# Optimization experiments

Measured on AMD Instinct MI355X. Metric: run time of the kernel, lower is better.

## Reference

```python
import jax, jax.numpy as jnp
import numpy as np

N, D, F, E, K = 8192, 1024, 4096, 8, 2


def setup_inputs() -> dict:
    key = jax.random.key(0)
    ks = jax.random.split(key, 4)
    x = jax.random.normal(ks[0], (N, D), dtype=jnp.float32)
    Wg = jax.random.normal(ks[1], (D, E), dtype=jnp.float32) * 0.02
    W1 = jax.random.normal(ks[2], (E, D, F), dtype=jnp.float32) * 0.02
    b1 = jnp.zeros((E, F), dtype=jnp.float32)
    W2 = jax.random.normal(ks[3], (E, F, D), dtype=jnp.float32) * 0.02
    b2 = jnp.zeros((E, D), dtype=jnp.float32)
    return {"x": x, "Wg": Wg, "W1": W1, "b1": b1, "W2": W2, "b2": b2}


def reference(x, Wg, W1, b1, W2, b2):
    # Top-k softmax gate (TopKGate): pick K experts per token, renormalize.
    logits = x @ Wg                                        # [N, E]
    probs = jax.nn.softmax(logits, axis=-1)
    gate_vals, expert_idx = jax.lax.top_k(probs, K)        # [N, K]
    gate_w = gate_vals / jnp.sum(gate_vals, axis=-1, keepdims=True)

    # Expert FFN (dispatch/combine math): the torch code sorts tokens by expert
    # id, all-to-alls them to the owning rank, applies the local Expert MLP,
    # and combines back weighted by gate_w. The jit-friendly equivalent is to
    # compute every expert's MLP for all tokens and gather the selected rows.
    h = jax.nn.relu(jnp.einsum('nd,edf->enf', x, W1) + b1[:, None, :])  # [E, N, F]
    o = jnp.einsum('enf,efd->end', h, W2) + b2[:, None, :]               # [E, N, D]

    tok = jnp.arange(x.shape[0])
    sel = o[expert_idx, tok[:, None]]                      # [N, K, D]
    y = jnp.sum(gate_w[..., None] * sel, axis=1)           # [N, D]
    return y
```

## Files before the change

kernel.cpp:

```cpp
#include <hip/hip_runtime.h>

#define N_TOK 8192
#define DIM   1024
#define FFN   4096
#define NEXP  8
#define TOPK  2
#define NENT  (N_TOK * TOPK)

using short8  = __attribute__((ext_vector_type(8))) short;
using floatx4 = __attribute__((ext_vector_type(4))) float;

__device__ __forceinline__ unsigned short f2bf(float f) {
    union { float f; unsigned u; } v; v.f = f;
    unsigned r = v.u + 0x7fffu + ((v.u >> 16) & 1u);
    return (unsigned short)(r >> 16);
}

#define GLOAD_LDS16(gptr, lptr) __builtin_amdgcn_global_load_lds( \
    (__attribute__((address_space(1))) void*)(void*)(gptr),       \
    (__attribute__((address_space(3))) void*)(lptr), 16, 0, 0)


__global__ __launch_bounds__(256) void cvt_x_kernel(const float4* __restrict__ in,
                                                    ushort4* __restrict__ out) {
    int i = blockIdx.x * 256 + threadIdx.x;
    float4 v = in[i];
    ushort4 o;
    o.x = f2bf(v.x); o.y = f2bf(v.y); o.z = f2bf(v.z); o.w = f2bf(v.w);
    out[i] = o;
}

__global__ __launch_bounds__(256) void transpose_cvt(const float* __restrict__ in,
                                                     unsigned short* __restrict__ out,
                                                     int R, int C) {
    __shared__ float tile[32][33];
    int e  = blockIdx.z;
    int c0 = blockIdx.x * 32;
    int r0 = blockIdx.y * 32;
    const float* inp = in + (size_t)e * R * C;
    unsigned short* outp = out + (size_t)e * R * C;
    int tx = threadIdx.x, ty = threadIdx.y;
#pragma unroll
    for (int i = 0; i < 4; i++) {
        int r = ty + i * 8;
        tile[r][tx] = inp[(size_t)(r0 + r) * C + c0 + tx];
    }
    __syncthreads();
#pragma unroll
    for (int i = 0; i < 4; i++) {
        int c = ty + i * 8;
        outp[(size_t)(c0 + c) * R + r0 + tx] = f2bf(tile[tx][c]);
    }
}


__global__ __launch_bounds__(256) void gating_kernel(const float* __restrict__ x,
                                                     const float* __restrict__ wg,
                                                     int* __restrict__ topk_e,
                                                     float* __restrict__ topk_w,
                                                     int* __restrict__ counts) {
    int wave = threadIdx.x >> 6, lane = threadIdx.x & 63;
    int t = blockIdx.x * 4 + wave;
    const float* xr = x + (size_t)t * DIM;
    float acc[NEXP];
#pragma unroll
    for (int e = 0; e < NEXP; e++) acc[e] = 0.f;
    for (int it = 0; it < DIM / 64; it++) {
        int d = it * 64 + lane;
        float xv = xr[d];
        const float4* wr = (const float4*)(wg + d * NEXP);
        float4 w0 = wr[0], w1 = wr[1];
        acc[0] += xv * w0.x; acc[1] += xv * w0.y; acc[2] += xv * w0.z; acc[3] += xv * w0.w;
        acc[4] += xv * w1.x; acc[5] += xv * w1.y; acc[6] += xv * w1.z; acc[7] += xv * w1.w;
    }
#pragma unroll
    for (int e = 0; e < NEXP; e++) {
#pragma unroll
        for (int off = 32; off > 0; off >>= 1) acc[e] += __shfl_xor(acc[e], off);
    }
    if (lane == 0) {
        int e1 = 0; float l1 = acc[0];
        for (int e = 1; e < NEXP; e++) if (acc[e] > l1) { l1 = acc[e]; e1 = e; }
        int e2 = -1; float l2 = -3.4e38f;
        for (int e = 0; e < NEXP; e++) if (e != e1 && acc[e] > l2) { l2 = acc[e]; e2 = e; }
        float w1v = 1.f / (1.f + expf(l2 - l1));
        topk_e[t * 2]     = e1;  topk_e[t * 2 + 1] = e2;
        topk_w[t * 2]     = w1v; topk_w[t * 2 + 1] = 1.f - w1v;
        atomicAdd(&counts[e1], 1);
        atomicAdd(&counts[e2], 1);
    }
}

__global__ void prefix_kernel(const int* __restrict__ counts, int* __restrict__ offs) {
    if (threadIdx.x == 0) {
        int s = 0;
        for (int e = 0; e < NEXP; e++) { offs[e] = s; s += counts[e]; }
        offs[NEXP] = s;
    }
}

__global__ __launch_bounds__(256) void scatter_kernel(const int* __restrict__ topk_e,
                                                      const float* __restrict__ topk_w,
                                                      const int* __restrict__ offs,
                                                      int* __restrict__ cursors,
                                                      int* __restrict__ entry_token,
                                                      float* __restrict__ entry_wgt) {
    int t = blockIdx.x * 256 + threadIdx.x;
#pragma unroll
    for (int k = 0; k < TOPK; k++) {
        int e = topk_e[t * 2 + k];
        int pos = offs[e] + atomicAdd(&cursors[e], 1);
        entry_token[pos] = t;
        entry_wgt[pos]  = topk_w[t * 2 + k];
    }
}


__global__ __launch_bounds__(256) void gemm1_kernel(
    const unsigned short* __restrict__ xb,
    const unsigned short* __restrict__ w1t,
    const float* __restrict__ b1,
    const int* __restrict__ offs,
    const int* __restrict__ entry_token,
    unsigned short* __restrict__ h)
{
    int e    = blockIdx.z;
    int base = offs[e];
    int cnt  = offs[e + 1] - base;
    int m0   = blockIdx.y * 128;
    if (m0 >= cnt) return;
    int f0   = blockIdx.x * 128;

    __shared__ unsigned short As[128 * 32];
    __shared__ unsigned short Bs[128 * 32];
    __shared__ int toks[128];

    int tid = threadIdx.x;
    if (tid < 128) {
        int r = m0 + tid;
        toks[tid] = entry_token[base + (r < cnt ? r : 0)];
    }
    __syncthreads();

    int wave = tid >> 6, lane = tid & 63;
    int wm = (wave >> 1) * 64, wn = (wave & 1) * 64;

    int rA   = wave * 32 + (lane >> 2);
    int colg = (lane & 3) * 8;
    const unsigned short* aG0 = xb + (size_t)toks[rA] * DIM + colg;
    const unsigned short* aG1 = xb + (size_t)toks[rA + 16] * DIM + colg;
    const unsigned short* bG0 = w1t + ((size_t)e * FFN + f0 + rA) * DIM + colg;
    const unsigned short* bG1 = bG0 + (size_t)16 * DIM;
    unsigned short* ldsA0 = &As[wave * 1024];
    unsigned short* ldsA1 = &As[wave * 1024 + 512];
    unsigned short* ldsB0 = &Bs[wave * 1024];
    unsigned short* ldsB1 = &Bs[wave * 1024 + 512];

    floatx4 acc[4][4];
#pragma unroll
    for (int i = 0; i < 4; i++)
#pragma unroll
        for (int j = 0; j < 4; j++) acc[i][j] = (floatx4)0.f;

    int quad = lane >> 4, rm = lane & 15;
    int aoff = (wm + rm) * 32 + quad * 8;
    int boff = (wn + rm) * 32 + quad * 8;

    for (int kk = 0; kk < DIM / 32; kk++) {
        GLOAD_LDS16(aG0, ldsA0);
        GLOAD_LDS16(aG1, ldsA1);
        GLOAD_LDS16(bG0, ldsB0);
        GLOAD_LDS16(bG1, ldsB1);
        aG0 += 32; aG1 += 32; bG0 += 32; bG1 += 32;
        __syncthreads();
        short8 af[4], bfr[4];
#pragma unroll
        for (int mi = 0; mi < 4; mi++) af[mi] = *(const short8*)&As[aoff + mi * 512];
#pragma unroll
        for (int ni = 0; ni < 4; ni++) bfr[ni] = *(const short8*)&Bs[boff + ni * 512];
#pragma unroll
        for (int mi = 0; mi < 4; mi++)
#pragma unroll
            for (int ni = 0; ni < 4; ni++)
                acc[mi][ni] = __builtin_amdgcn_mfma_f32_16x16x32_bf16(af[mi], bfr[ni], acc[mi][ni], 0, 0, 0);
        __syncthreads();
    }

#pragma unroll
    for (int mi = 0; mi < 4; mi++) {
        int mbase = wm + mi * 16 + quad * 4;
#pragma unroll
        for (int ni = 0; ni < 4; ni++) {
            int f = f0 + wn + ni * 16 + rm;
            float bias = b1[e * FFN + f];
            floatx4 v = acc[mi][ni];
#pragma unroll
            for (int r = 0; r < 4; r++) {
                int row = m0 + mbase + r;
                if (row < cnt) {
                    float t = v[r] + bias;
                    t = t > 0.f ? t : 0.f;
                    h[(size_t)(base + row) * FFN + f] = f2bf(t);
                }
            }
        }
    }
}


__global__ __launch_bounds__(256) void gemm2_kernel(
    const unsigned short* __restrict__ h,
    const unsigned short* __restrict__ w2t,
    const float* __restrict__ b2,
    const int* __restrict__ offs,
    const int* __restrict__ entry_token,
    const float* __restrict__ entry_wgt,
    float* __restrict__ y)
{
    int e    = blockIdx.z;
    int base = offs[e];
    int cnt  = offs[e + 1] - base;
    int m0   = blockIdx.y * 128;
    if (m0 >= cnt) return;
    int n0   = blockIdx.x * 128;

    __shared__ unsigned short As[128 * 32];
    __shared__ unsigned short Bs[128 * 32];

    int tid = threadIdx.x;
    int wave = tid >> 6, lane = tid & 63;
    int wm = (wave >> 1) * 64, wn = (wave & 1) * 64;

    int rA   = wave * 32 + (lane >> 2);
    int colg = (lane & 3) * 8;
    const unsigned short* aG0 = h + (size_t)(base + m0 + rA) * FFN + colg;
    const unsigned short* aG1 = aG0 + (size_t)16 * FFN;
    const unsigned short* bG0 = w2t + ((size_t)e * DIM + n0 + rA) * FFN + colg;
    const unsigned short* bG1 = bG0 + (size_t)16 * FFN;
    unsigned short* ldsA0 = &As[wave * 1024];
    unsigned short* ldsA1 = &As[wave * 1024 + 512];
    unsigned short* ldsB0 = &Bs[wave * 1024];
    unsigned short* ldsB1 = &Bs[wave * 1024 + 512];

    floatx4 acc[4][4];
#pragma unroll
    for (int i = 0; i < 4; i++)
#pragma unroll
        for (int j = 0; j < 4; j++) acc[i][j] = (floatx4)0.f;

    int quad = lane >> 4, rm = lane & 15;
    int aoff = (wm + rm) * 32 + quad * 8;
    int boff = (wn + rm) * 32 + quad * 8;

    for (int kk = 0; kk < FFN / 32; kk++) {
        GLOAD_LDS16(aG0, ldsA0);
        GLOAD_LDS16(aG1, ldsA1);
        GLOAD_LDS16(bG0, ldsB0);
        GLOAD_LDS16(bG1, ldsB1);
        aG0 += 32; aG1 += 32; bG0 += 32; bG1 += 32;
        __syncthreads();
        short8 af[4], bfr[4];
#pragma unroll
        for (int mi = 0; mi < 4; mi++) af[mi] = *(const short8*)&As[aoff + mi * 512];
#pragma unroll
        for (int ni = 0; ni < 4; ni++) bfr[ni] = *(const short8*)&Bs[boff + ni * 512];
#pragma unroll
        for (int mi = 0; mi < 4; mi++)
#pragma unroll
            for (int ni = 0; ni < 4; ni++)
                acc[mi][ni] = __builtin_amdgcn_mfma_f32_16x16x32_bf16(af[mi], bfr[ni], acc[mi][ni], 0, 0, 0);
        __syncthreads();
    }

#pragma unroll
    for (int mi = 0; mi < 4; mi++) {
        int mbase = wm + mi * 16 + quad * 4;
#pragma unroll
        for (int ni = 0; ni < 4; ni++) {
            int n = n0 + wn + ni * 16 + rm;
            float bias = b2[e * DIM + n];
            floatx4 v = acc[mi][ni];
#pragma unroll
            for (int r = 0; r < 4; r++) {
                int row = m0 + mbase + r;
                if (row < cnt) {
                    int   tok = entry_token[base + row];
                    float w   = entry_wgt[base + row];
                    atomicAdd(&y[(size_t)tok * DIM + n], (v[r] + bias) * w);
                }
            }
        }
    }
}


extern "C" void kernel_launch(void* const* d_in, const int* in_sizes, int n_in,
                              void* d_out, int out_size, void* d_ws, size_t ws_size,
                              hipStream_t stream) {
    const float* x  = (const float*)d_in[0];
    const float* Wg = (const float*)d_in[1];
    const float* W1 = (const float*)d_in[2];
    const float* b1 = (const float*)d_in[3];
    const float* W2 = (const float*)d_in[4];
    const float* b2 = (const float*)d_in[5];
    float* y = (float*)d_out;

    char* p = (char*)d_ws;
    unsigned short* xb  = (unsigned short*)p; p += (size_t)N_TOK * DIM * 2;
    unsigned short* w1t = (unsigned short*)p; p += (size_t)NEXP * DIM * FFN * 2;
    unsigned short* w2t = (unsigned short*)p; p += (size_t)NEXP * DIM * FFN * 2;
    unsigned short* h   = (unsigned short*)p; p += (size_t)(NENT + 128) * FFN * 2;
    int*   topk_e      = (int*)p;   p += (size_t)N_TOK * TOPK * 4;
    float* topk_w      = (float*)p; p += (size_t)N_TOK * TOPK * 4;
    int*   entry_token = (int*)p;   p += (size_t)NENT * 4;
    float* entry_wgt   = (float*)p; p += (size_t)NENT * 4;
    int*   counts      = (int*)p;   p += NEXP * 4;
    int*   cursors     = (int*)p;   p += NEXP * 4;
    int*   offs        = (int*)p;   p += (NEXP + 1) * 4;

    hipMemsetAsync(d_out, 0, (size_t)out_size * 4, stream);
    hipMemsetAsync(counts, 0, NEXP * 4 * 2, stream);

    cvt_x_kernel<<<(N_TOK * DIM) / (256 * 4), 256, 0, stream>>>((const float4*)x, (ushort4*)xb);
    transpose_cvt<<<dim3(FFN / 32, DIM / 32, NEXP), dim3(32, 8), 0, stream>>>(W1, w1t, DIM, FFN);
    transpose_cvt<<<dim3(DIM / 32, FFN / 32, NEXP), dim3(32, 8), 0, stream>>>(W2, w2t, FFN, DIM);
    gating_kernel<<<N_TOK / 4, 256, 0, stream>>>(x, Wg, topk_e, topk_w, counts);
    prefix_kernel<<<1, 64, 0, stream>>>(counts, offs);
    scatter_kernel<<<N_TOK / 256, 256, 0, stream>>>(topk_e, topk_w, offs, cursors, entry_token, entry_wgt);
    gemm1_kernel<<<dim3(FFN / 128, 64, NEXP), 256, 0, stream>>>(xb, w1t, b1, offs, entry_token, h);
    gemm2_kernel<<<dim3(DIM / 128, 64, NEXP), 256, 0, stream>>>(h, w2t, b2, offs, entry_token, entry_wgt, y);
}
```

Measured before the change: 1.128 ms.

## Double K-tile depth to 64 with XOR-swizzled LDS layout in both expert GEMMs

Both expert GEMMs now stage a 64-wide K slice per iteration instead of 32, which halves the number of barrier pairs per tile. The LDS layout uses an XOR swizzle on 16-byte chunks so the MFMA fragment reads avoid bank conflicts. The weight transpose kernel now handles 64 rows per block and writes packed ushort2 stores for wider writes. This costs twice the LDS per block, which may lower occupancy.

```diff
diff --git a/kernel.cpp b/kernel.cpp
--- a/kernel.cpp
+++ b/kernel.cpp
@@ -33,23 +33,26 @@
 __global__ __launch_bounds__(256) void transpose_cvt(const float* __restrict__ in,
                                                      unsigned short* __restrict__ out,
                                                      int R, int C) {
-    __shared__ float tile[32][33];
+    __shared__ float tile[64][33];
     int e  = blockIdx.z;
     int c0 = blockIdx.x * 32;
-    int r0 = blockIdx.y * 32;
+    int r0 = blockIdx.y * 64;
     const float* inp = in + (size_t)e * R * C;
     unsigned short* outp = out + (size_t)e * R * C;
     int tx = threadIdx.x, ty = threadIdx.y;
 #pragma unroll
+    for (int i = 0; i < 8; i++) {
+        int r = i * 8 + ty;
+        tile[r][tx] = inp[(size_t)(r0 + r) * C + c0 + tx];
+    }
+    __syncthreads();
+#pragma unroll
     for (int i = 0; i < 4; i++) {
-        int r = ty + i * 8;
-        tile[r][tx] = inp[(size_t)(r0 + r) * C + c0 + tx];
-    }
-    __syncthreads();
-#pragma unroll
-    for (int i = 0; i < 4; i++) {
-        int c = ty + i * 8;
-        outp[(size_t)(c0 + c) * R + r0 + tx] = f2bf(tile[tx][c]);
+        int c = i * 8 + ty;
+        ushort2 v;
+        v.x = f2bf(tile[2 * tx][c]);
+        v.y = f2bf(tile[2 * tx + 1][c]);
+        *(ushort2*)&outp[(size_t)(c0 + c) * R + r0 + 2 * tx] = v;
     }
 }
 
@@ -131,8 +134,8 @@
     if (m0 >= cnt) return;
     int f0   = blockIdx.x * 128;
 
-    __shared__ unsigned short As[128 * 32];
-    __shared__ unsigned short Bs[128 * 32];
+    __shared__ unsigned short As[128 * 64];
+    __shared__ unsigned short Bs[128 * 64];
     __shared__ int toks[128];
 
     int tid = threadIdx.x;
@@ -145,16 +148,20 @@
     int wave = tid >> 6, lane = tid & 63;
     int wm = (wave >> 1) * 64, wn = (wave & 1) * 64;
 
-    int rA   = wave * 32 + (lane >> 2);
-    int colg = (lane & 3) * 8;
-    const unsigned short* aG0 = xb + (size_t)toks[rA] * DIM + colg;
-    const unsigned short* aG1 = xb + (size_t)toks[rA + 16] * DIM + colg;
-    const unsigned short* bG0 = w1t + ((size_t)e * FFN + f0 + rA) * DIM + colg;
-    const unsigned short* bG1 = bG0 + (size_t)16 * DIM;
-    unsigned short* ldsA0 = &As[wave * 1024];
-    unsigned short* ldsA1 = &As[wave * 1024 + 512];
-    unsigned short* ldsB0 = &Bs[wave * 1024];
-    unsigned short* ldsB1 = &Bs[wave * 1024 + 512];
+    int r8 = lane >> 3, sc = lane & 7;
+    const unsigned short* aG[4];
+    const unsigned short* bG[4];
+    unsigned short* ldsA[4];
+    unsigned short* ldsB[4];
+#pragma unroll
+    for (int l = 0; l < 4; l++) {
+        int row = wave * 32 + l * 8 + r8;
+        int g16 = sc ^ (row & 7);
+        aG[l] = xb + (size_t)toks[row] * DIM + g16 * 8;
+        bG[l] = w1t + ((size_t)e * FFN + f0 + row) * DIM + g16 * 8;
+        ldsA[l] = &As[(wave * 32 + l * 8) * 64];
+        ldsB[l] = &Bs[(wave * 32 + l * 8) * 64];
+    }
 
     floatx4 acc[4][4];
 #pragma unroll
@@ -163,26 +170,33 @@
         for (int j = 0; j < 4; j++) acc[i][j] = (floatx4)0.f;
 
     int quad = lane >> 4, rm = lane & 15;
-    int aoff = (wm + rm) * 32 + quad * 8;
-    int boff = (wn + rm) * 32 + quad * 8;
-
-    for (int kk = 0; kk < DIM / 32; kk++) {
-        GLOAD_LDS16(aG0, ldsA0);
-        GLOAD_LDS16(aG1, ldsA1);
-        GLOAD_LDS16(bG0, ldsB0);
-        GLOAD_LDS16(bG1, ldsB1);
-        aG0 += 32; aG1 += 32; bG0 += 32; bG1 += 32;
+    int sw = rm & 7;
+
+    for (int kk = 0; kk < DIM / 64; kk++) {
+#pragma unroll
+        for (int l = 0; l < 4; l++) {
+            GLOAD_LDS16(aG[l], ldsA[l]);
+            GLOAD_LDS16(bG[l], ldsB[l]);
+        }
+#pragma unroll
+        for (int l = 0; l < 4; l++) { aG[l] += 64; bG[l] += 64; }
         __syncthreads();
-        short8 af[4], bfr[4];
-#pragma unroll
-        for (int mi = 0; mi < 4; mi++) af[mi] = *(const short8*)&As[aoff + mi * 512];
-#pragma unroll
-        for (int ni = 0; ni < 4; ni++) bfr[ni] = *(const short8*)&Bs[boff + ni * 512];
-#pragma unroll
-        for (int mi = 0; mi < 4; mi++)
+#pragma unroll
+        for (int k2 = 0; k2 < 2; k2++) {
+            int c16 = (k2 * 4 + quad) ^ sw;
+            short8 af[4], bfr[4];
+#pragma unroll
+            for (int mi = 0; mi < 4; mi++)
+                af[mi] = *(const short8*)&As[(wm + mi * 16 + rm) * 64 + c16 * 8];
 #pragma unroll
             for (int ni = 0; ni < 4; ni++)
-                acc[mi][ni] = __builtin_amdgcn_mfma_f32_16x16x32_bf16(af[mi], bfr[ni], acc[mi][ni], 0, 0, 0);
+                bfr[ni] = *(const short8*)&Bs[(wn + ni * 16 + rm) * 64 + c16 * 8];
+#pragma unroll
+            for (int mi = 0; mi < 4; mi++)
+#pragma unroll
+                for (int ni = 0; ni < 4; ni++)
+                    acc[mi][ni] = __builtin_amdgcn_mfma_f32_16x16x32_bf16(af[mi], bfr[ni], acc[mi][ni], 0, 0, 0);
+        }
         __syncthreads();
     }
 
@@ -224,23 +238,27 @@
     if (m0 >= cnt) return;
     int n0   = blockIdx.x * 128;
 
-    __shared__ unsigned short As[128 * 32];
-    __shared__ unsigned short Bs[128 * 32];
+    __shared__ unsigned short As[128 * 64];
+    __shared__ unsigned short Bs[128 * 64];
 
     int tid = threadIdx.x;
     int wave = tid >> 6, lane = tid & 63;
     int wm = (wave >> 1) * 64, wn = (wave & 1) * 64;
 
-    int rA   = wave * 32 + (lane >> 2);
-    int colg = (lane & 3) * 8;
-    const unsigned short* aG0 = h + (size_t)(base + m0 + rA) * FFN + colg;
-    const unsigned short* aG1 = aG0 + (size_t)16 * FFN;
-    const unsigned short* bG0 = w2t + ((size_t)e * DIM + n0 + rA) * FFN + colg;
-    const unsigned short* bG1 = bG0 + (size_t)16 * FFN;
-    unsigned short* ldsA0 = &As[wave * 1024];
-    unsigned short* ldsA1 = &As[wave * 1024 + 512];
-    unsigned short* ldsB0 = &Bs[wave * 1024];
-    unsigned short* ldsB1 = &Bs[wave * 1024 + 512];
+    int r8 = lane >> 3, sc = lane & 7;
+    const unsigned short* aG[4];
+    const unsigned short* bG[4];
+    unsigned short* ldsA[4];
+    unsigned short* ldsB[4];
+#pragma unroll
+    for (int l = 0; l < 4; l++) {
+        int row = wave * 32 + l * 8 + r8;
+        int g16 = sc ^ (row & 7);
+        aG[l] = h + (size_t)(base + m0 + row) * FFN + g16 * 8;
+        bG[l] = w2t + ((size_t)e * DIM + n0 + row) * FFN + g16 * 8;
+        ldsA[l] = &As[(wave * 32 + l * 8) * 64];
+        ldsB[l] = &Bs[(wave * 32 + l * 8) * 64];
+    }
 
     floatx4 acc[4][4];
 #pragma unroll
@@ -249,26 +267,33 @@
         for (int j = 0; j < 4; j++) acc[i][j] = (floatx4)0.f;
 
     int quad = lane >> 4, rm = lane & 15;
-    int aoff = (wm + rm) * 32 + quad * 8;
-    int boff = (wn + rm) * 32 + quad * 8;
-
-    for (int kk = 0; kk < FFN / 32; kk++) {
-        GLOAD_LDS16(aG0, ldsA0);
-        GLOAD_LDS16(aG1, ldsA1);
-        GLOAD_LDS16(bG0, ldsB0);
-        GLOAD_LDS16(bG1, ldsB1);
-        aG0 += 32; aG1 += 32; bG0 += 32; bG1 += 32;
+    int sw = rm & 7;
+
+    for (int kk = 0; kk < FFN / 64; kk++) {
+#pragma unroll
+        for (int l = 0; l < 4; l++) {
+            GLOAD_LDS16(aG[l], ldsA[l]);
+            GLOAD_LDS16(bG[l], ldsB[l]);
+        }
+#pragma unroll
+        for (int l = 0; l < 4; l++) { aG[l] += 64; bG[l] += 64; }
         __syncthreads();
-        short8 af[4], bfr[4];
-#pragma unroll
-        for (int mi = 0; mi < 4; mi++) af[mi] = *(const short8*)&As[aoff + mi * 512];
-#pragma unroll
-        for (int ni = 0; ni < 4; ni++) bfr[ni] = *(const short8*)&Bs[boff + ni * 512];
-#pragma unroll
-        for (int mi = 0; mi < 4; mi++)
+#pragma unroll
+        for (int k2 = 0; k2 < 2; k2++) {
+            int c16 = (k2 * 4 + quad) ^ sw;
+            short8 af[4], bfr[4];
+#pragma unroll
+            for (int mi = 0; mi < 4; mi++)
+                af[mi] = *(const short8*)&As[(wm + mi * 16 + rm) * 64 + c16 * 8];
 #pragma unroll
             for (int ni = 0; ni < 4; ni++)
-                acc[mi][ni] = __builtin_amdgcn_mfma_f32_16x16x32_bf16(af[mi], bfr[ni], acc[mi][ni], 0, 0, 0);
+                bfr[ni] = *(const short8*)&Bs[(wn + ni * 16 + rm) * 64 + c16 * 8];
+#pragma unroll
+            for (int mi = 0; mi < 4; mi++)
+#pragma unroll
+                for (int ni = 0; ni < 4; ni++)
+                    acc[mi][ni] = __builtin_amdgcn_mfma_f32_16x16x32_bf16(af[mi], bfr[ni], acc[mi][ni], 0, 0, 0);
+        }
         __syncthreads();
     }
 
@@ -322,8 +347,8 @@
     hipMemsetAsync(counts, 0, NEXP * 4 * 2, stream);
 
     cvt_x_kernel<<<(N_TOK * DIM) / (256 * 4), 256, 0, stream>>>((const float4*)x, (ushort4*)xb);
-    transpose_cvt<<<dim3(FFN / 32, DIM / 32, NEXP), dim3(32, 8), 0, stream>>>(W1, w1t, DIM, FFN);
-    transpose_cvt<<<dim3(DIM / 32, FFN / 32, NEXP), dim3(32, 8), 0, stream>>>(W2, w2t, FFN, DIM);
+    transpose_cvt<<<dim3(FFN / 32, DIM / 64, NEXP), dim3(32, 8), 0, stream>>>(W1, w1t, DIM, FFN);
+    transpose_cvt<<<dim3(DIM / 32, FFN / 64, NEXP), dim3(32, 8), 0, stream>>>(W2, w2t, FFN, DIM);
     gating_kernel<<<N_TOK / 4, 256, 0, stream>>>(x, Wg, topk_e, topk_w, counts);
     prefix_kernel<<<1, 64, 0, stream>>>(counts, offs);
     scatter_kernel<<<N_TOK / 256, 256, 0, stream>>>(topk_e, topk_w, offs, cursors, entry_token, entry_wgt);
```

Measured after the change: 1.203 ms. 6.6% more time.

## Swizzle LDS tiles, interleave experts in grid, widen weight transpose tiles

Applied to the files above, without the earlier changes.

The GEMM kernels now XOR-swizzle the 16-byte column chunks of each LDS row, both on the global-to-LDS load and on the fragment reads. This is meant to remove LDS bank conflicts when reading MFMA fragments. The grid is flattened to 1D with the expert index in the low bits, so early-exiting blocks for empty M tiles are spread across experts and the dispatch is better balanced. The weight transpose/convert kernel moves to 64x64 tiles with vectorized ushort4 stores to cut per-block overhead and widen writes.

```diff
diff --git a/kernel.cpp b/kernel.cpp
--- a/kernel.cpp
+++ b/kernel.cpp
@@ -33,23 +33,30 @@
 __global__ __launch_bounds__(256) void transpose_cvt(const float* __restrict__ in,
                                                      unsigned short* __restrict__ out,
                                                      int R, int C) {
-    __shared__ float tile[32][33];
+    __shared__ float tile[64][65];
     int e  = blockIdx.z;
-    int c0 = blockIdx.x * 32;
-    int r0 = blockIdx.y * 32;
+    int c0 = blockIdx.x * 64;
+    int r0 = blockIdx.y * 64;
     const float* inp = in + (size_t)e * R * C;
     unsigned short* outp = out + (size_t)e * R * C;
-    int tx = threadIdx.x, ty = threadIdx.y;
+    int tid = threadIdx.x;
+    int lrow = tid >> 6, lcol = tid & 63;
+#pragma unroll
+    for (int i = 0; i < 16; i++) {
+        int r = i * 4 + lrow;
+        tile[r][lcol] = inp[(size_t)(r0 + r) * C + c0 + lcol];
+    }
+    __syncthreads();
+    int r4 = (tid & 15) * 4;
 #pragma unroll
     for (int i = 0; i < 4; i++) {
-        int r = ty + i * 8;
-        tile[r][tx] = inp[(size_t)(r0 + r) * C + c0 + tx];
-    }
-    __syncthreads();
-#pragma unroll
-    for (int i = 0; i < 4; i++) {
-        int c = ty + i * 8;
-        outp[(size_t)(c0 + c) * R + r0 + tx] = f2bf(tile[tx][c]);
+        int c = i * 16 + (tid >> 4);
+        ushort4 o;
+        o.x = f2bf(tile[r4 + 0][c]);
+        o.y = f2bf(tile[r4 + 1][c]);
+        o.z = f2bf(tile[r4 + 2][c]);
+        o.w = f2bf(tile[r4 + 3][c]);
+        *(ushort4*)&outp[(size_t)(c0 + c) * R + r0 + r4] = o;
     }
 }
 
@@ -124,12 +131,16 @@
     const int* __restrict__ entry_token,
     unsigned short* __restrict__ h)
 {
-    int e    = blockIdx.z;
+    int bid  = blockIdx.x;
+    int e    = bid & 7;
+    int slot = bid >> 3;
+    int mt   = slot & 63;
+    int nt   = slot >> 6;
     int base = offs[e];
     int cnt  = offs[e + 1] - base;
-    int m0   = blockIdx.y * 128;
+    int m0   = mt * 128;
     if (m0 >= cnt) return;
-    int f0   = blockIdx.x * 128;
+    int f0   = nt * 128;
 
     __shared__ unsigned short As[128 * 32];
     __shared__ unsigned short Bs[128 * 32];
@@ -145,16 +156,20 @@
     int wave = tid >> 6, lane = tid & 63;
     int wm = (wave >> 1) * 64, wn = (wave & 1) * 64;
 
-    int rA   = wave * 32 + (lane >> 2);
-    int colg = (lane & 3) * 8;
-    const unsigned short* aG0 = xb + (size_t)toks[rA] * DIM + colg;
-    const unsigned short* aG1 = xb + (size_t)toks[rA + 16] * DIM + colg;
-    const unsigned short* bG0 = w1t + ((size_t)e * FFN + f0 + rA) * DIM + colg;
-    const unsigned short* bG1 = bG0 + (size_t)16 * DIM;
-    unsigned short* ldsA0 = &As[wave * 1024];
-    unsigned short* ldsA1 = &As[wave * 1024 + 512];
-    unsigned short* ldsB0 = &Bs[wave * 1024];
-    unsigned short* ldsB1 = &Bs[wave * 1024 + 512];
+    int lr = lane >> 2, sl = lane & 3;
+    int g0 = (sl ^ ((lr >> 1) & 3)) * 8;
+    const unsigned short* aG[2];
+    const unsigned short* bG[2];
+    unsigned short* ldsA[2];
+    unsigned short* ldsB[2];
+#pragma unroll
+    for (int c = 0; c < 2; c++) {
+        int row = wave * 32 + c * 16 + lr;
+        aG[c] = xb + (size_t)toks[row] * DIM + g0;
+        bG[c] = w1t + ((size_t)e * FFN + f0 + row) * DIM + g0;
+        ldsA[c] = &As[(wave * 32 + c * 16) * 32];
+        ldsB[c] = &Bs[(wave * 32 + c * 16) * 32];
+    }
 
     floatx4 acc[4][4];
 #pragma unroll
@@ -163,21 +178,22 @@
         for (int j = 0; j < 4; j++) acc[i][j] = (floatx4)0.f;
 
     int quad = lane >> 4, rm = lane & 15;
-    int aoff = (wm + rm) * 32 + quad * 8;
-    int boff = (wn + rm) * 32 + quad * 8;
+    int slf  = (quad ^ ((rm >> 1) & 3)) * 8;
+    int arow = (wm + rm) * 32;
+    int brow = (wn + rm) * 32;
 
     for (int kk = 0; kk < DIM / 32; kk++) {
-        GLOAD_LDS16(aG0, ldsA0);
-        GLOAD_LDS16(aG1, ldsA1);
-        GLOAD_LDS16(bG0, ldsB0);
-        GLOAD_LDS16(bG1, ldsB1);
-        aG0 += 32; aG1 += 32; bG0 += 32; bG1 += 32;
+        GLOAD_LDS16(aG[0], ldsA[0]);
+        GLOAD_LDS16(aG[1], ldsA[1]);
+        GLOAD_LDS16(bG[0], ldsB[0]);
+        GLOAD_LDS16(bG[1], ldsB[1]);
+        aG[0] += 32; aG[1] += 32; bG[0] += 32; bG[1] += 32;
         __syncthreads();
         short8 af[4], bfr[4];
 #pragma unroll
-        for (int mi = 0; mi < 4; mi++) af[mi] = *(const short8*)&As[aoff + mi * 512];
-#pragma unroll
-        for (int ni = 0; ni < 4; ni++) bfr[ni] = *(const short8*)&Bs[boff + ni * 512];
+        for (int mi = 0; mi < 4; mi++) af[mi] = *(const short8*)&As[arow + mi * 512 + slf];
+#pragma unroll
+        for (int ni = 0; ni < 4; ni++) bfr[ni] = *(const short8*)&Bs[brow + ni * 512 + slf];
 #pragma unroll
         for (int mi = 0; mi < 4; mi++)
 #pragma unroll
@@ -217,12 +233,16 @@
     const float* __restrict__ entry_wgt,
     float* __restrict__ y)
 {
-    int e    = blockIdx.z;
+    int bid  = blockIdx.x;
+    int e    = bid & 7;
+    int slot = bid >> 3;
+    int mt   = slot & 63;
+    int nt   = slot >> 6;
     int base = offs[e];
     int cnt  = offs[e + 1] - base;
-    int m0   = blockIdx.y * 128;
+    int m0   = mt * 128;
     if (m0 >= cnt) return;
-    int n0   = blockIdx.x * 128;
+    int n0   = nt * 128;
 
     __shared__ unsigned short As[128 * 32];
     __shared__ unsigned short Bs[128 * 32];
@@ -231,16 +251,20 @@
     int wave = tid >> 6, lane = tid & 63;
     int wm = (wave >> 1) * 64, wn = (wave & 1) * 64;
 
-    int rA   = wave * 32 + (lane >> 2);
-    int colg = (lane & 3) * 8;
-    const unsigned short* aG0 = h + (size_t)(base + m0 + rA) * FFN + colg;
-    const unsigned short* aG1 = aG0 + (size_t)16 * FFN;
-    const unsigned short* bG0 = w2t + ((size_t)e * DIM + n0 + rA) * FFN + colg;
-    const unsigned short* bG1 = bG0 + (size_t)16 * FFN;
-    unsigned short* ldsA0 = &As[wave * 1024];
-    unsigned short* ldsA1 = &As[wave * 1024 + 512];
-    unsigned short* ldsB0 = &Bs[wave * 1024];
-    unsigned short* ldsB1 = &Bs[wave * 1024 + 512];
+    int lr = lane >> 2, sl = lane & 3;
+    int g0 = (sl ^ ((lr >> 1) & 3)) * 8;
+    const unsigned short* aG[2];
+    const unsigned short* bG[2];
+    unsigned short* ldsA[2];
+    unsigned short* ldsB[2];
+#pragma unroll
+    for (int c = 0; c < 2; c++) {
+        int row = wave * 32 + c * 16 + lr;
+        aG[c] = h + (size_t)(base + m0 + row) * FFN + g0;
+        bG[c] = w2t + ((size_t)e * DIM + n0 + row) * FFN + g0;
+        ldsA[c] = &As[(wave * 32 + c * 16) * 32];
+        ldsB[c] = &Bs[(wave * 32 + c * 16) * 32];
+    }
 
     floatx4 acc[4][4];
 #pragma unroll
@@ -249,21 +273,22 @@
         for (int j = 0; j < 4; j++) acc[i][j] = (floatx4)0.f;
 
     int quad = lane >> 4, rm = lane & 15;
-    int aoff = (wm + rm) * 32 + quad * 8;
-    int boff = (wn + rm) * 32 + quad * 8;
+    int slf  = (quad ^ ((rm >> 1) & 3)) * 8;
+    int arow = (wm + rm) * 32;
+    int brow = (wn + rm) * 32;
 
     for (int kk = 0; kk < FFN / 32; kk++) {
-        GLOAD_LDS16(aG0, ldsA0);
-        GLOAD_LDS16(aG1, ldsA1);
-        GLOAD_LDS16(bG0, ldsB0);
-        GLOAD_LDS16(bG1, ldsB1);
-        aG0 += 32; aG1 += 32; bG0 += 32; bG1 += 32;
+        GLOAD_LDS16(aG[0], ldsA[0]);
+        GLOAD_LDS16(aG[1], ldsA[1]);
+        GLOAD_LDS16(bG[0], ldsB[0]);
+        GLOAD_LDS16(bG[1], ldsB[1]);
+        aG[0] += 32; aG[1] += 32; bG[0] += 32; bG[1] += 32;
         __syncthreads();
         short8 af[4], bfr[4];
 #pragma unroll
-        for (int mi = 0; mi < 4; mi++) af[mi] = *(const short8*)&As[aoff + mi * 512];
-#pragma unroll
-        for (int ni = 0; ni < 4; ni++) bfr[ni] = *(const short8*)&Bs[boff + ni * 512];
+        for (int mi = 0; mi < 4; mi++) af[mi] = *(const short8*)&As[arow + mi * 512 + slf];
+#pragma unroll
+        for (int ni = 0; ni < 4; ni++) bfr[ni] = *(const short8*)&Bs[brow + ni * 512 + slf];
 #pragma unroll
         for (int mi = 0; mi < 4; mi++)
 #pragma unroll
@@ -322,11 +347,11 @@
     hipMemsetAsync(counts, 0, NEXP * 4 * 2, stream);
 
     cvt_x_kernel<<<(N_TOK * DIM) / (256 * 4), 256, 0, stream>>>((const float4*)x, (ushort4*)xb);
-    transpose_cvt<<<dim3(FFN / 32, DIM / 32, NEXP), dim3(32, 8), 0, stream>>>(W1, w1t, DIM, FFN);
-    transpose_cvt<<<dim3(DIM / 32, FFN / 32, NEXP), dim3(32, 8), 0, stream>>>(W2, w2t, FFN, DIM);
+    transpose_cvt<<<dim3(FFN / 64, DIM / 64, NEXP), 256, 0, stream>>>(W1, w1t, DIM, FFN);
+    transpose_cvt<<<dim3(DIM / 64, FFN / 64, NEXP), 256, 0, stream>>>(W2, w2t, FFN, DIM);
     gating_kernel<<<N_TOK / 4, 256, 0, stream>>>(x, Wg, topk_e, topk_w, counts);
     prefix_kernel<<<1, 64, 0, stream>>>(counts, offs);
     scatter_kernel<<<N_TOK / 256, 256, 0, stream>>>(topk_e, topk_w, offs, cursors, entry_token, entry_wgt);
-    gemm1_kernel<<<dim3(FFN / 128, 64, NEXP), 256, 0, stream>>>(xb, w1t, b1, offs, entry_token, h);
-    gemm2_kernel<<<dim3(DIM / 128, 64, NEXP), 256, 0, stream>>>(h, w2t, b2, offs, entry_token, entry_wgt, y);
-}
+    gemm1_kernel<<<NEXP * 64 * 32, 256, 0, stream>>>(xb, w1t, b1, offs, entry_token, h);
+    gemm2_kernel<<<NEXP * 64 * 8, 256, 0, stream>>>(h, w2t, b2, offs, entry_token, entry_wgt, y);
+}
```

Result: no change. 1.119 ms (-0.9%).
